# Kernel tuning notes

Measured on AMD Instinct MI355X. Metric: run time of the kernel, lower is better.

## Reference

```python
import jax, jax.numpy as jnp
import numpy as np

N = 16384
NUM_GRAPHS = 512
CUTOFF = 5.0
MAX_NEIGHBORS = 32


def setup_inputs() -> dict:
    key = jax.random.key(0)
    k1, k2 = jax.random.split(key)
    pos = jax.random.normal(k1, (N, 3), dtype=jnp.float32)
    batch = jnp.sort(jax.random.randint(k2, (N,), 0, NUM_GRAPHS)).astype(jnp.int32)
    return {"pos": pos, "batch": batch}


def reference(pos, batch):
    """radius_graph(pos, r=CUTOFF, batch=batch, max_num_neighbors=K) + edge norms.

    Static-shape formulation: each target node gets exactly K neighbor slots
    (its K nearest in-radius, same-graph, non-self neighbors); invalid slots are
    padded as self-loops with weight 0 and flagged by `edge_mask`.
    Returns (edge_index [2, N*K], edge_weight [N*K], edge_mask [N*K]).
    """
    K = MAX_NEIGHBORS
    n = pos.shape[0]
    BIG = jnp.float32(1e30)

    # Pairwise squared distances via the Gram trick (avoids [N,N,3]).
    sq = jnp.sum(pos * pos, axis=-1)                      # [N]
    d2 = sq[:, None] + sq[None, :] - 2.0 * (pos @ pos.T)  # [N,N]
    d2 = jnp.maximum(d2, 0.0)

    idx_n = jnp.arange(n)
    valid = (batch[:, None] == batch[None, :]) \
            & (idx_n[:, None] != idx_n[None, :]) \
            & (d2 <= CUTOFF * CUTOFF)
    d2m = jnp.where(valid, d2, BIG)

    # K nearest valid neighbors per target node (row = target i).
    neg_d2, nbr = jax.lax.top_k(-d2m, K)                  # [N,K]
    edge_mask = (-neg_d2) < (BIG * 0.5)                   # [N,K] valid slots

    col = jnp.broadcast_to(idx_n[:, None], (n, K))        # target node i
    row = jnp.where(edge_mask, nbr, col)                  # source j (pad = self)

    row_f = row.reshape(-1)
    col_f = col.reshape(-1)
    m = edge_mask.reshape(-1)

    diff = pos[row_f] - pos[col_f]                        # [N*K, 3]
    sqd = jnp.sum(diff * diff, axis=-1)
    edge_weight = jnp.sqrt(jnp.where(m, sqd, 1.0)) * m.astype(pos.dtype)

    edge_index = jnp.stack([row_f, col_f])                # [2, N*K]
    return edge_index, edge_weight, m
```

## Files before the change

kernel.cpp:

```cpp
#include <hip/hip_runtime.h>
#include <hip/hip_bf16.h>
#include <stdint.h>

#define NN   16384
#define KK   32
#define NKE  (NN * KK)

__device__ __forceinline__ int wave_lower_bound(const int* __restrict__ batch,
                                                int n, int v, int lane) {
    int s = 0, e = n;
    while (e - s > 1) {
        int L    = e - s;
        int step = (L + 63) >> 6;
        long idx = (long)s + (long)lane * (long)step;
        bool pred = (idx < (long)e) && (batch[idx] < v);
        unsigned long long m = __ballot(pred);
        int c = __popcll(m);
        int ns = (c > 0) ? (s + (c - 1) * step + 1) : s;
        long net = (long)s + (long)c * (long)step;
        int ne = (c < 64 && net < (long)e) ? (int)net : e;
        s = ns; e = ne;
        if (s > e) s = e;
    }
    if (e > s && batch[s] < v) s = e;
    return s;
}

__device__ __forceinline__ void bitonic_sort64_u32(unsigned& key, int lane) {
    for (int k = 2; k <= 64; k <<= 1) {
        for (int j = k >> 1; j >= 1; j >>= 1) {
            unsigned other = __shfl_xor(key, j);
            bool keep_min = (((lane & j) == 0) == ((lane & k) == 0));
            unsigned mn = key < other ? key : other;
            unsigned mx = key < other ? other : key;
            key = keep_min ? mn : mx;
        }
    }
}

__device__ __forceinline__ void bitonic_merge64_u32(unsigned& key, int lane) {
    for (int j = 32; j >= 1; j >>= 1) {
        unsigned other = __shfl_xor(key, j);
        bool keep_min = ((lane & j) == 0);
        unsigned mn = key < other ? key : other;
        unsigned mx = key < other ? other : key;
        key = keep_min ? mn : mx;
    }
}

__global__ __launch_bounds__(256, 8)
void radius_graph_kernel(const float* __restrict__ pos,
                         const int*   __restrict__ batch,
                         float* __restrict__ out) {
    int tid  = threadIdx.x;
    int lane = tid & 63;
    int i = __builtin_amdgcn_readfirstlane((blockIdx.x * 256 + tid) >> 6);

    int b = batch[i];

    int idx0 = i - 64 + lane;
    int v0   = batch[idx0 < 0 ? 0 : idx0];
    int idx1 = i + lane;
    int v1   = batch[idx1 >= NN ? NN - 1 : idx1];

    unsigned long long m0 = __ballot(idx0 >= 0 && v0 == b);
    int cnt_lo = (m0 == ~0ull) ? 64 : __clzll(~m0);
    unsigned long long m1 = __ballot(idx1 < NN && v1 == b);
    unsigned long long nm1 = ~m1;
    int cnt_hi = (nm1 == 0ull) ? 64 : (__ffsll(nm1) - 1);

    int lo, hi;
    if (cnt_lo < 64 && cnt_hi < 64) {
        lo = i - cnt_lo;
        hi = i + cnt_hi;
    } else {
        lo = wave_lower_bound(batch, NN, b, lane);
        hi = wave_lower_bound(batch, NN, b + 1, lane);
    }

    float xi = pos[3 * i + 0];
    float yi = pos[3 * i + 1];
    float zi = pos[3 * i + 2];
    float sqi = __fadd_rn(__fadd_rn(__fmul_rn(xi, xi), __fmul_rn(yi, yi)),
                          __fmul_rn(zi, zi));

    auto key_for = [&](int j) -> unsigned {
        if (j >= hi || j == i) return ~0u;
        float xj = pos[3 * j + 0];
        float yj = pos[3 * j + 1];
        float zj = pos[3 * j + 2];
        float sqj = __fadd_rn(__fadd_rn(__fmul_rn(xj, xj), __fmul_rn(yj, yj)),
                              __fmul_rn(zj, zj));
        float dot = __fadd_rn(__fadd_rn(__fmul_rn(xi, xj), __fmul_rn(yi, yj)),
                              __fmul_rn(zi, zj));
        float d2 = __fsub_rn(__fadd_rn(sqi, sqj), __fmul_rn(2.0f, dot));
        d2 = fmaxf(d2, 0.0f);
        if (!(d2 <= 25.0f)) return ~0u;
        return (__float_as_uint(d2) & 0xFFFFC000u) | (unsigned)j;
    };

    unsigned key = key_for(lo + lane);
    bitonic_sort64_u32(key, lane);

    for (int base = lo + 64; base < hi; base += 64) {
        unsigned k2 = key_for(base + lane);
        bitonic_sort64_u32(k2, lane);
        unsigned rev = __shfl(k2, 63 - lane);
        key = (key < rev) ? key : rev;
        bitonic_merge64_u32(key, lane);
    }

    int s = lane & 31;
    unsigned ks = __shfl(key, s);
    bool valid = (ks != ~0u);
    int e = i * KK + s;

    if (lane < 32) {
        int row = valid ? (int)(ks & 0x3FFFu) : i;
        out[e] = (float)row;
        float d2s = __uint_as_float(ks & 0xFFFFC000u);
        out[2 * NKE + e] = valid ? sqrtf(d2s) : 0.0f;
    } else {
        out[NKE + e]     = (float)i;
        out[3 * NKE + e] = valid ? 1.0f : 0.0f;
    }
}

extern "C" void kernel_launch(void* const* d_in, const int* in_sizes, int n_in,
                              void* d_out, int out_size, void* d_ws, size_t ws_size,
                              hipStream_t stream) {
    const float* pos   = (const float*)d_in[0];
    const int*   batch = (const int*)d_in[1];
    float* out = (float*)d_out;

    dim3 block(256);
    dim3 grid((NN * 64) / 256);
    radius_graph_kernel<<<grid, block, 0, stream>>>(pos, batch, out);
}
```

Before: 12.34 us.

## Process two target nodes per wavefront using 32-lane half-wave bitonic sorts

Each 64-lane wavefront now handles two consecutive target nodes, one per 32-lane half. Each half runs its own 32-element bitonic sort and merge over its candidate chunk, and the graph bounds for both nodes are derived from shared ballots. The intent is to halve the number of wavefronts and the shuffle-heavy sort work per node, since only K=32 results are needed. Each half now loops over the larger of the two spans and needs twice as many chunk iterations, and all four outputs are written directly from each half.

```diff
diff --git a/kernel.cpp b/kernel.cpp
--- a/kernel.cpp
+++ b/kernel.cpp
@@ -1,5 +1,4 @@
 #include <hip/hip_runtime.h>
-#include <hip/hip_bf16.h>
 #include <stdint.h>
 
 #define NN   16384
@@ -26,11 +25,11 @@
     return s;
 }
 
-__device__ __forceinline__ void bitonic_sort64_u32(unsigned& key, int lane) {
-    for (int k = 2; k <= 64; k <<= 1) {
+__device__ __forceinline__ void bitonic_sort32_half(unsigned& key, int sub) {
+    for (int k = 2; k <= 32; k <<= 1) {
         for (int j = k >> 1; j >= 1; j >>= 1) {
             unsigned other = __shfl_xor(key, j);
-            bool keep_min = (((lane & j) == 0) == ((lane & k) == 0));
+            bool keep_min = (((sub & j) == 0) == ((sub & k) == 0));
             unsigned mn = key < other ? key : other;
             unsigned mx = key < other ? other : key;
             key = keep_min ? mn : mx;
@@ -38,10 +37,10 @@
     }
 }
 
-__device__ __forceinline__ void bitonic_merge64_u32(unsigned& key, int lane) {
-    for (int j = 32; j >= 1; j >>= 1) {
+__device__ __forceinline__ void bitonic_merge32_half(unsigned& key, int sub) {
+    for (int j = 16; j >= 1; j >>= 1) {
         unsigned other = __shfl_xor(key, j);
-        bool keep_min = ((lane & j) == 0);
+        bool keep_min = ((sub & j) == 0);
         unsigned mn = key < other ? key : other;
         unsigned mx = key < other ? other : key;
         key = keep_min ? mn : mx;
@@ -54,29 +53,49 @@
                          float* __restrict__ out) {
     int tid  = threadIdx.x;
     int lane = tid & 63;
-    int i = __builtin_amdgcn_readfirstlane((blockIdx.x * 256 + tid) >> 6);
+    int sub  = lane & 31;
+    int half = lane >> 5;
+    int w    = blockIdx.x * 4 + (tid >> 6);
+    int i0   = 2 * w;
+    int i    = i0 + half;
 
-    int b = batch[i];
-
-    int idx0 = i - 64 + lane;
+    int idx0 = i0 - 64 + lane;
     int v0   = batch[idx0 < 0 ? 0 : idx0];
-    int idx1 = i + lane;
+    int idx1 = i0 + lane;
     int v1   = batch[idx1 >= NN ? NN - 1 : idx1];
 
-    unsigned long long m0 = __ballot(idx0 >= 0 && v0 == b);
+    int b0 = __shfl(v1, 0);
+    int b1 = __shfl(v1, 1);
+
+    unsigned long long m0 = __ballot(idx0 >= 0 && v0 == b0);
     int cnt_lo = (m0 == ~0ull) ? 64 : __clzll(~m0);
-    unsigned long long m1 = __ballot(idx1 < NN && v1 == b);
+    unsigned long long m1 = __ballot(idx1 < NN && v1 == b0);
     unsigned long long nm1 = ~m1;
     int cnt_hi = (nm1 == 0ull) ? 64 : (__ffsll(nm1) - 1);
 
-    int lo, hi;
-    if (cnt_lo < 64 && cnt_hi < 64) {
-        lo = i - cnt_lo;
-        hi = i + cnt_hi;
+    unsigned long long m1b = __ballot(idx1 < NN && v1 == b1);
+    unsigned long long t = ~(m1b >> 1);
+    int r1 = __ffsll(t) - 1;
+
+    int lo0, hi0, lo1, hi1;
+    bool edge0 = (cnt_lo >= 64) || (cnt_hi >= 64);
+    bool edge1 = (b1 != b0) && (r1 >= 63);
+    if (!edge0 && !edge1) {
+        lo0 = i0 - cnt_lo;
+        hi0 = i0 + cnt_hi;
+        if (b1 == b0) { lo1 = lo0; hi1 = hi0; }
+        else          { lo1 = i0 + 1; hi1 = i0 + 1 + r1; }
     } else {
-        lo = wave_lower_bound(batch, NN, b, lane);
-        hi = wave_lower_bound(batch, NN, b + 1, lane);
+        lo0 = wave_lower_bound(batch, NN, b0, lane);
+        hi0 = wave_lower_bound(batch, NN, b0 + 1, lane);
+        if (b1 == b0) { lo1 = lo0; hi1 = hi0; }
+        else {
+            lo1 = wave_lower_bound(batch, NN, b1, lane);
+            hi1 = wave_lower_bound(batch, NN, b1 + 1, lane);
+        }
     }
+    int lo = half ? lo1 : lo0;
+    int hi = half ? hi1 : hi0;
 
     float xi = pos[3 * i + 0];
     float yi = pos[3 * i + 1];
@@ -99,31 +118,26 @@
         return (__float_as_uint(d2) & 0xFFFFC000u) | (unsigned)j;
     };
 
-    unsigned key = key_for(lo + lane);
-    bitonic_sort64_u32(key, lane);
+    unsigned key = key_for(lo + sub);
+    bitonic_sort32_half(key, sub);
 
-    for (int base = lo + 64; base < hi; base += 64) {
-        unsigned k2 = key_for(base + lane);
-        bitonic_sort64_u32(k2, lane);
-        unsigned rev = __shfl(k2, 63 - lane);
+    int span = (hi0 - lo0 > hi1 - lo1) ? (hi0 - lo0) : (hi1 - lo1);
+    for (int off = 32; off < span; off += 32) {
+        unsigned k2 = key_for(lo + off + sub);
+        bitonic_sort32_half(k2, sub);
+        unsigned rev = __shfl(k2, (lane & 32) | (31 - sub));
         key = (key < rev) ? key : rev;
-        bitonic_merge64_u32(key, lane);
+        bitonic_merge32_half(key, sub);
     }
 
-    int s = lane & 31;
-    unsigned ks = __shfl(key, s);
-    bool valid = (ks != ~0u);
-    int e = i * KK + s;
-
-    if (lane < 32) {
-        int row = valid ? (int)(ks & 0x3FFFu) : i;
-        out[e] = (float)row;
-        float d2s = __uint_as_float(ks & 0xFFFFC000u);
-        out[2 * NKE + e] = valid ? sqrtf(d2s) : 0.0f;
-    } else {
-        out[NKE + e]     = (float)i;
-        out[3 * NKE + e] = valid ? 1.0f : 0.0f;
-    }
+    bool valid = (key != ~0u);
+    int e = i * KK + sub;
+    int rowj = valid ? (int)(key & 0x3FFFu) : i;
+    out[e]           = (float)rowj;
+    out[NKE + e]     = (float)i;
+    float d2s = __uint_as_float(key & 0xFFFFC000u);
+    out[2 * NKE + e] = valid ? sqrtf(d2s) : 0.0f;
+    out[3 * NKE + e] = valid ? 1.0f : 0.0f;
 }
 
 extern "C" void kernel_launch(void* const* d_in, const int* in_sizes, int n_in,
@@ -134,6 +148,6 @@
     float* out = (float*)d_out;
 
     dim3 block(256);
-    dim3 grid((NN * 64) / 256);
+    dim3 grid((NN / 2 * 64) / 256);
     radius_graph_kernel<<<grid, block, 0, stream>>>(pos, batch, out);
 }
```

Measured after the change: 11.57 us. 6.3% less time.
